# Performance work log

Measured on AMD Instinct MI355X. Metric: run time of the kernel, lower is better.

The kernel has to match this reference:

```python
import jax, jax.numpy as jnp
import numpy as np

B, S, IN, HID, NH, HD, R, WIN, TK = 2, 2048, 64, 512, 8, 64, 64, 5, 16
C1, C2, C3 = 171, 171, 170  # hidden_dim split across 3 conv branches (512 = 171+171+170)


def _conv(xc, w, b, pad):
    y = jax.lax.conv_general_dilated(xc, w, window_strides=(1,), padding=[(pad, pad)],
                                     dimension_numbers=('NCH', 'OIH', 'NCH'))
    return jax.nn.relu(y + b[None, :, None])


def setup_inputs():
    key = jax.random.key(0)
    ks = jax.random.split(key, 22)
    p = lambda k, sh: jax.random.normal(k, sh, jnp.float32) * 0.05
    return {
        'x': jax.random.normal(ks[0], (B, S, IN), jnp.float32),
        'conv1_w': p(ks[1], (C1, IN, 3)), 'conv1_b': p(ks[2], (C1,)),
        'conv2_w': p(ks[3], (C2, IN, 5)), 'conv2_b': p(ks[4], (C2,)),
        'conv3_w': p(ks[5], (C3, IN, 7)), 'conv3_b': p(ks[6], (C3,)),
        'Wq': p(ks[7], (HID, HID)), 'bq': p(ks[8], (HID,)),
        'Wk': p(ks[9], (HID, HID)), 'bk': p(ks[10], (HID,)),
        'Wv': p(ks[11], (HID, HID)), 'bv': p(ks[12], (HID,)),
        'Wkp': p(ks[13], (R, HD)), 'bkp': p(ks[14], (R,)),
        'Wvp': p(ks[15], (R, HD)), 'bvp': p(ks[16], (R,)),
        'Wo': p(ks[17], (HID, HID)), 'bo': p(ks[18], (HID,)),
        'ln_g': jnp.ones((HID,), jnp.float32), 'ln_b': jnp.zeros((HID,), jnp.float32),
    }


def reference(x, conv1_w, conv1_b, conv2_w, conv2_b, conv3_w, conv3_b,
              Wq, bq, Wk, bk, Wv, bv, Wkp, bkp, Wvp, bvp, Wo, bo, ln_g, ln_b):
    # multi-scale conv front-end
    xc = x.transpose(0, 2, 1)  # [B, IN, S]
    h = jnp.concatenate([_conv(xc, conv1_w, conv1_b, 1),
                         _conv(xc, conv2_w, conv2_b, 2),
                         _conv(xc, conv3_w, conv3_b, 3)], axis=1).transpose(0, 2, 1)  # [B,S,HID]

    def heads(W_, b_):
        return (h @ W_.T + b_).reshape(B, S, NH, HD).transpose(0, 2, 1, 3)  # [B,NH,S,HD]

    Q, K, V = heads(Wq, bq), heads(Wk, bk), heads(Wv, bv)
    Kp = K @ Wkp.T + bkp  # [B,NH,S,R]
    Vp = V @ Wvp.T + bvp

    # local sliding-window attention; -inf masking reproduces the per-t boundary slicing
    hw = WIN // 2
    idx = jnp.arange(S)[:, None] + jnp.arange(-hw, hw + 1)[None, :]
    valid = (idx >= 0) & (idx < S)
    idxc = jnp.clip(idx, 0, S - 1)
    Kw = K[:, :, idxc, :]
    Vw = V[:, :, idxc, :]
    ls = jnp.einsum('bhsd,bhswd->bhsw', Q, Kw) / jnp.sqrt(jnp.float32(HD))
    ls = jnp.where(valid[None, None], ls, -jnp.inf)
    local = jnp.einsum('bhsw,bhswd->bhsd', jax.nn.softmax(ls, axis=-1), Vw)

    # top-k low-rank global attention (HD == R required by original einsum)
    gs = jnp.einsum('bhqd,bhkd->bhqk', Q, Kp) / jnp.sqrt(jnp.float32(R))  # [B,NH,S,S]
    tv, ti = jax.lax.top_k(gs, TK)
    tw = jax.nn.softmax(tv, axis=-1)  # [B,NH,S,TK]
    bi = jnp.arange(B)[:, None, None, None]
    hi = jnp.arange(NH)[None, :, None, None]
    topV = Vp[bi, hi, ti]  # [B,NH,S,TK,R]
    sp = jnp.einsum('bhqk,bhqkr->bhqr', tw, topV)
    sp = sp @ Wvp.T + bvp  # extra value_proj applied to sparse output, as in original

    out = ((local + sp) * 0.5).transpose(0, 2, 1, 3).reshape(B, S, HID)
    out = out @ Wo.T + bo
    res = out + h
    mu = res.mean(-1, keepdims=True)
    var = ((res - mu) ** 2).mean(-1, keepdims=True)
    return (res - mu) / jnp.sqrt(var + 1e-5) * ln_g + ln_b
```

## Files before the change

kernel.cpp:

```cpp
#include <hip/hip_runtime.h>
#include <hip/hip_bf16.h>

#define BB 2
#define SS 2048
#define INC 64
#define HIDN 512
#define NHH 8
#define HDD 64
#define SP 2054

typedef __attribute__((ext_vector_type(8))) short bf16x8;
typedef __attribute__((ext_vector_type(4))) float f32x4;

__device__ __forceinline__ short f2bf(float f) {
  union { __hip_bfloat16 h; short s; } u;
  u.h = __float2bfloat16(f);
  return u.s;
}
__device__ __forceinline__ float bf2f(short s) {
  return __uint_as_float(((unsigned)(unsigned short)s) << 16);
}

__global__ __launch_bounds__(256) void prep_kernel(
    const float* __restrict__ x, const float* __restrict__ w1,
    const float* __restrict__ b1, const float* __restrict__ w2,
    const float* __restrict__ b2, const float* __restrict__ w3,
    const float* __restrict__ b3, const float* __restrict__ Wq,
    const float* __restrict__ Wk_, const float* __restrict__ Wv_,
    const float* __restrict__ bq, const float* __restrict__ bk_,
    const float* __restrict__ bv_, const float* __restrict__ Wo,
    const float* __restrict__ Wkp, const float* __restrict__ Wvp,
    const float* __restrict__ bvp, short* __restrict__ Wallbf,
    float* __restrict__ ball, short* __restrict__ Wobf,
    short* __restrict__ Wkpbf, short* __restrict__ W2bf,
    float* __restrict__ cvec, short* __restrict__ xbfp,
    short* __restrict__ Wcbf, float* __restrict__ bcat) {
  int i0 = blockIdx.x * 256 + threadIdx.x;
  int stride = gridDim.x * 256;
  for (int idx = i0; idx < 786432; idx += stride) {
    float v;
    if (idx < 262144)      v = Wq[idx];
    else if (idx < 524288) v = Wk_[idx - 262144];
    else                   v = Wv_[idx - 524288];
    Wallbf[idx] = f2bf(v);
  }
  for (int idx = i0; idx < 262144; idx += stride) Wobf[idx] = f2bf(Wo[idx]);
  for (int idx = i0; idx < BB * SP * 64; idx += stride) {
    int row = idx >> 6, ci = idx & 63;
    int b = row / SP, pr = row - b * SP;
    int sg = pr - 3;
    float v = (sg >= 0 && sg < SS) ? x[(b * SS + sg) * 64 + ci] : 0.f;
    xbfp[idx] = f2bf(v);
  }
  for (int idx = i0; idx < 512 * 448; idx += stride) {
    int c = idx / 448;
    int rem = idx - c * 448;
    int t = rem >> 6, ci = rem & 63;
    float v = 0.f;
    if (c < 171) {
      int k = t - 2;
      if (k >= 0 && k < 3) v = w1[(c * 64 + ci) * 3 + k];
    } else if (c < 342) {
      int k = t - 1;
      if (k >= 0 && k < 5) v = w2[((c - 171) * 64 + ci) * 5 + k];
    } else {
      v = w3[((c - 342) * 64 + ci) * 7 + t];
    }
    Wcbf[idx] = f2bf(v);
  }
  for (int idx = i0; idx < 4096; idx += stride) {
    Wkpbf[idx] = f2bf(Wkp[idx]);
    int j = idx >> 6, d = idx & 63;
    float s = 0.f;
#pragma unroll 8
    for (int i = 0; i < 64; i++) s += Wvp[j * 64 + i] * Wvp[i * 64 + d];
    W2bf[idx] = f2bf(s);
  }
  if (i0 < 1536) {
    float v;
    if (i0 < 512)       v = bq[i0];
    else if (i0 < 1024) v = bk_[i0 - 512];
    else                v = bv_[i0 - 1024];
    ball[i0] = v;
  }
  if (i0 < 512) {
    float v;
    if (i0 < 171)      v = b1[i0];
    else if (i0 < 342) v = b2[i0 - 171];
    else               v = b3[i0 - 342];
    bcat[i0] = v;
  }
  if (i0 < 64) {
    float s = bvp[i0];
#pragma unroll 8
    for (int i = 0; i < 64; i++) s += bvp[i] * Wvp[i0 * 64 + i];
    cvec[i0] = s;
  }
}

__global__ __launch_bounds__(256, 4) void gemm_conv(
    const short* __restrict__ xbfp, const short* __restrict__ Wcbf,
    const float* __restrict__ bcat, short* __restrict__ hbf) {
  int m0 = blockIdx.x * 128;
  int n0 = blockIdx.y * 64;
  int tid = threadIdx.x;
  int wvv = tid >> 6, lane = tid & 63;
  int quad = lane >> 4, l16 = lane & 15;
  int mw = m0 + wvv * 32;
  int r0 = mw + l16, r1 = r0 + 16;
  int b0 = r0 >> 11, s0 = r0 & 2047;
  int b1 = r1 >> 11, s1 = r1 & 2047;
  const short* ap0 = xbfp + (size_t)(b0 * SP + s0) * 64 + quad * 8;
  const short* ap1 = xbfp + (size_t)(b1 * SP + s1) * 64 + quad * 8;
  const short* bp = Wcbf + (size_t)(n0 + l16) * 448 + quad * 8;
  f32x4 acc[2][4] = {};
  bf16x8 cA0 = *(const bf16x8*)ap0;
  bf16x8 cA1 = *(const bf16x8*)ap1;
  bf16x8 cB0 = *(const bf16x8*)(bp + 0 * 16 * 448);
  bf16x8 cB1 = *(const bf16x8*)(bp + 1 * 16 * 448);
  bf16x8 cB2 = *(const bf16x8*)(bp + 2 * 16 * 448);
  bf16x8 cB3 = *(const bf16x8*)(bp + 3 * 16 * 448);
#pragma unroll 2
  for (int ks = 0; ks < 14; ks++) {
    int offn = (ks + 1 < 14 ? ks + 1 : 13) * 32;
    bf16x8 nA0 = *(const bf16x8*)(ap0 + offn);
    bf16x8 nA1 = *(const bf16x8*)(ap1 + offn);
    bf16x8 nB0 = *(const bf16x8*)(bp + 0 * 16 * 448 + offn);
    bf16x8 nB1 = *(const bf16x8*)(bp + 1 * 16 * 448 + offn);
    bf16x8 nB2 = *(const bf16x8*)(bp + 2 * 16 * 448 + offn);
    bf16x8 nB3 = *(const bf16x8*)(bp + 3 * 16 * 448 + offn);
    acc[0][0] = __builtin_amdgcn_mfma_f32_16x16x32_bf16(cA0, cB0, acc[0][0], 0, 0, 0);
    acc[1][0] = __builtin_amdgcn_mfma_f32_16x16x32_bf16(cA1, cB0, acc[1][0], 0, 0, 0);
    acc[0][1] = __builtin_amdgcn_mfma_f32_16x16x32_bf16(cA0, cB1, acc[0][1], 0, 0, 0);
    acc[1][1] = __builtin_amdgcn_mfma_f32_16x16x32_bf16(cA1, cB1, acc[1][1], 0, 0, 0);
    acc[0][2] = __builtin_amdgcn_mfma_f32_16x16x32_bf16(cA0, cB2, acc[0][2], 0, 0, 0);
    acc[1][2] = __builtin_amdgcn_mfma_f32_16x16x32_bf16(cA1, cB2, acc[1][2], 0, 0, 0);
    acc[0][3] = __builtin_amdgcn_mfma_f32_16x16x32_bf16(cA0, cB3, acc[0][3], 0, 0, 0);
    acc[1][3] = __builtin_amdgcn_mfma_f32_16x16x32_bf16(cA1, cB3, acc[1][3], 0, 0, 0);
    cA0 = nA0; cA1 = nA1;
    cB0 = nB0; cB1 = nB1; cB2 = nB2; cB3 = nB3;
  }
#pragma unroll
  for (int mt = 0; mt < 2; mt++) {
#pragma unroll
    for (int r = 0; r < 4; r++) {
      int m = mw + mt * 16 + quad * 4 + r;
#pragma unroll
      for (int t = 0; t < 4; t++) {
        int n = n0 + t * 16 + l16;
        float v = fmaxf(acc[mt][t][r] + bcat[n], 0.f);
        hbf[(size_t)m * 512 + n] = f2bf(v);
      }
    }
  }
}

__global__ __launch_bounds__(256, 4) void gemm_qkv(
    const short* __restrict__ Abf, const short* __restrict__ Wbf,
    const float* __restrict__ bias, short* __restrict__ Qh,
    short* __restrict__ Kh, short* __restrict__ Vh) {
  int m0 = blockIdx.x * 128;
  int n0 = blockIdx.y * 64;
  int tid = threadIdx.x;
  int wvv = tid >> 6, lane = tid & 63;
  int quad = lane >> 4, l16 = lane & 15;
  int mw = m0 + wvv * 32;
  const short* ap0 = Abf + (size_t)(mw + l16) * 512 + quad * 8;
  const short* ap1 = ap0 + 16 * 512;
  const short* bp = Wbf + (size_t)(n0 + l16) * 512 + quad * 8;
  f32x4 acc[2][4] = {};
  bf16x8 cA0 = *(const bf16x8*)ap0;
  bf16x8 cA1 = *(const bf16x8*)ap1;
  bf16x8 cB0 = *(const bf16x8*)(bp + 0 * 16 * 512);
  bf16x8 cB1 = *(const bf16x8*)(bp + 1 * 16 * 512);
  bf16x8 cB2 = *(const bf16x8*)(bp + 2 * 16 * 512);
  bf16x8 cB3 = *(const bf16x8*)(bp + 3 * 16 * 512);
#pragma unroll 2
  for (int ks = 0; ks < 16; ks++) {
    int offn = (ks + 1 < 16 ? ks + 1 : 15) * 32;
    bf16x8 nA0 = *(const bf16x8*)(ap0 + offn);
    bf16x8 nA1 = *(const bf16x8*)(ap1 + offn);
    bf16x8 nB0 = *(const bf16x8*)(bp + 0 * 16 * 512 + offn);
    bf16x8 nB1 = *(const bf16x8*)(bp + 1 * 16 * 512 + offn);
    bf16x8 nB2 = *(const bf16x8*)(bp + 2 * 16 * 512 + offn);
    bf16x8 nB3 = *(const bf16x8*)(bp + 3 * 16 * 512 + offn);
    acc[0][0] = __builtin_amdgcn_mfma_f32_16x16x32_bf16(cA0, cB0, acc[0][0], 0, 0, 0);
    acc[1][0] = __builtin_amdgcn_mfma_f32_16x16x32_bf16(cA1, cB0, acc[1][0], 0, 0, 0);
    acc[0][1] = __builtin_amdgcn_mfma_f32_16x16x32_bf16(cA0, cB1, acc[0][1], 0, 0, 0);
    acc[1][1] = __builtin_amdgcn_mfma_f32_16x16x32_bf16(cA1, cB1, acc[1][1], 0, 0, 0);
    acc[0][2] = __builtin_amdgcn_mfma_f32_16x16x32_bf16(cA0, cB2, acc[0][2], 0, 0, 0);
    acc[1][2] = __builtin_amdgcn_mfma_f32_16x16x32_bf16(cA1, cB2, acc[1][2], 0, 0, 0);
    acc[0][3] = __builtin_amdgcn_mfma_f32_16x16x32_bf16(cA0, cB3, acc[0][3], 0, 0, 0);
    acc[1][3] = __builtin_amdgcn_mfma_f32_16x16x32_bf16(cA1, cB3, acc[1][3], 0, 0, 0);
    cA0 = nA0; cA1 = nA1;
    cB0 = nB0; cB1 = nB1; cB2 = nB2; cB3 = nB3;
  }
  int which = n0 >> 9;
  int head = (n0 >> 6) & 7;
  short* dst = which == 0 ? Qh : (which == 1 ? Kh : Vh);
  float scale = which == 0 ? 0.125f : 1.0f;
#pragma unroll
  for (int mt = 0; mt < 2; mt++) {
#pragma unroll
    for (int r = 0; r < 4; r++) {
      int m = mw + mt * 16 + quad * 4 + r;
      int bb = m >> 11, s = m & 2047;
      size_t rowoff = ((size_t)(bb * 8 + head) * 2048 + s) * 64;
#pragma unroll
      for (int t = 0; t < 4; t++) {
        int hd = t * 16 + l16;
        float v = acc[mt][t][r] + bias[n0 + hd];
        dst[rowoff + hd] = f2bf(v * scale);
      }
    }
  }
}

__global__ __launch_bounds__(256, 4) void kpvp_local_kernel(
    const short* __restrict__ Kh, const short* __restrict__ Vh,
    const short* __restrict__ Wkpbf, const float* __restrict__ bkp,
    const short* __restrict__ W2bf, const float* __restrict__ cvec,
    short* __restrict__ Kfrag, float* __restrict__ Vpp,
    const short* __restrict__ Qh, float* __restrict__ ctxl) {
  int tid = threadIdx.x;
  __shared__ float Sloc[4][2][16][17];
  __shared__ float wloc[4][16][8];
  if (blockIdx.x < 256) {
    int m0 = blockIdx.x * 128;
    int wvv = tid >> 6, lane = tid & 63;
    int quad = lane >> 4, l16 = lane & 15;
    int mw = m0 + wvv * 32;
    {
      const short* ap0 = Kh + (size_t)(mw + l16) * 64 + quad * 8;
      const short* ap1 = ap0 + 16 * 64;
      const short* bp = Wkpbf + l16 * 64 + quad * 8;
      bf16x8 A00 = *(const bf16x8*)ap0, A01 = *(const bf16x8*)(ap0 + 32);
      bf16x8 A10 = *(const bf16x8*)ap1, A11 = *(const bf16x8*)(ap1 + 32);
      f32x4 acc[2][4] = {};
#pragma unroll
      for (int t = 0; t < 4; t++) {
        bf16x8 B0 = *(const bf16x8*)(bp + t * 16 * 64);
        bf16x8 B1 = *(const bf16x8*)(bp + t * 16 * 64 + 32);
        acc[0][t] = __builtin_amdgcn_mfma_f32_16x16x32_bf16(A00, B0, acc[0][t], 0, 0, 0);
        acc[0][t] = __builtin_amdgcn_mfma_f32_16x16x32_bf16(A01, B1, acc[0][t], 0, 0, 0);
        acc[1][t] = __builtin_amdgcn_mfma_f32_16x16x32_bf16(A10, B0, acc[1][t], 0, 0, 0);
        acc[1][t] = __builtin_amdgcn_mfma_f32_16x16x32_bf16(A11, B1, acc[1][t], 0, 0, 0);
      }
#pragma unroll
      for (int mt = 0; mt < 2; mt++)
#pragma unroll
        for (int r = 0; r < 4; r++) {
          int m = mw + mt * 16 + quad * 4 + r;
          int m15 = m & 15;
          size_t gbase = (size_t)(m >> 4) * 1024;
#pragma unroll
          for (int t = 0; t < 4; t++) {
            int n = t * 16 + l16;
            short val = f2bf(acc[mt][t][r] + bkp[n]);
            Kfrag[gbase + (size_t)(n >> 5) * 512 +
                  ((((n & 31) >> 3) * 16 + m15) << 3) + (n & 7)] = val;
          }
        }
    }
    {
      const short* ap0 = Vh + (size_t)(mw + l16) * 64 + quad * 8;
      const short* ap1 = ap0 + 16 * 64;
      const short* bp = W2bf + l16 * 64 + quad * 8;
      bf16x8 A00 = *(const bf16x8*)ap0, A01 = *(const bf16x8*)(ap0 + 32);
      bf16x8 A10 = *(const bf16x8*)ap1, A11 = *(const bf16x8*)(ap1 + 32);
      f32x4 acc[2][4] = {};
#pragma unroll
      for (int t = 0; t < 4; t++) {
        bf16x8 B0 = *(const bf16x8*)(bp + t * 16 * 64);
        bf16x8 B1 = *(const bf16x8*)(bp + t * 16 * 64 + 32);
        acc[0][t] = __builtin_amdgcn_mfma_f32_16x16x32_bf16(A00, B0, acc[0][t], 0, 0, 0);
        acc[0][t] = __builtin_amdgcn_mfma_f32_16x16x32_bf16(A01, B1, acc[0][t], 0, 0, 0);
        acc[1][t] = __builtin_amdgcn_mfma_f32_16x16x32_bf16(A10, B0, acc[1][t], 0, 0, 0);
        acc[1][t] = __builtin_amdgcn_mfma_f32_16x16x32_bf16(A11, B1, acc[1][t], 0, 0, 0);
      }
#pragma unroll
      for (int mt = 0; mt < 2; mt++)
#pragma unroll
        for (int r = 0; r < 4; r++) {
          int m = mw + mt * 16 + quad * 4 + r;
#pragma unroll
          for (int t = 0; t < 4; t++) {
            int n = t * 16 + l16;
            Vpp[(size_t)m * 64 + n] = acc[mt][t][r] + cvec[n];
          }
        }
    }
    return;
  }
  int wv = tid >> 6;
  int tile = (blockIdx.x - 256) * 4 + wv;
  int bh = tile >> 7;
  int q0 = (tile & 127) * 16;
  int lane = tid & 63;
  int quad = lane >> 4, l16 = lane & 15;

  const short* qbase = Qh + (size_t)(bh * 2048 + q0 + l16) * 64 + quad * 8;
  bf16x8 a0 = *(const bf16x8*)qbase;
  bf16x8 a1 = *(const bf16x8*)(qbase + 32);

  int k0a = min(max(q0 - 2 + l16, 0), 2047);
  int k1a = min(q0 + 6 + l16, 2047);
  const short* kb0 = Kh + (size_t)(bh * 2048 + k0a) * 64 + quad * 8;
  const short* kb1 = Kh + (size_t)(bh * 2048 + k1a) * 64 + quad * 8;
  bf16x8 B00 = *(const bf16x8*)kb0;
  bf16x8 B01 = *(const bf16x8*)(kb0 + 32);
  bf16x8 B10 = *(const bf16x8*)kb1;
  bf16x8 B11 = *(const bf16x8*)(kb1 + 32);
  f32x4 C0 = {0.f, 0.f, 0.f, 0.f};
  f32x4 C1 = {0.f, 0.f, 0.f, 0.f};
  C0 = __builtin_amdgcn_mfma_f32_16x16x32_bf16(a0, B00, C0, 0, 0, 0);
  C0 = __builtin_amdgcn_mfma_f32_16x16x32_bf16(a1, B01, C0, 0, 0, 0);
  C1 = __builtin_amdgcn_mfma_f32_16x16x32_bf16(a0, B10, C1, 0, 0, 0);
  C1 = __builtin_amdgcn_mfma_f32_16x16x32_bf16(a1, B11, C1, 0, 0, 0);
#pragma unroll
  for (int r = 0; r < 4; r++) {
    Sloc[wv][0][quad * 4 + r][l16] = C0[r];
    Sloc[wv][1][quad * 4 + r][l16] = C1[r];
  }
  __builtin_amdgcn_wave_barrier();
  if (lane < 16) {
    int q = lane;
    float sc[5];
    bool ok[5];
#pragma unroll
    for (int j = 0; j < 5; j++) {
      int offq = q + j - 2;
      int sg = q0 + offq;
      ok[j] = (sg >= 0 && sg < SS);
      int t = offq <= 13 ? 0 : 1;
      int col = t ? offq - 6 : offq + 2;
      sc[j] = ok[j] ? Sloc[wv][t][q][col] : -3.0e38f;
    }
    float m = -3.0e38f;
#pragma unroll
    for (int j = 0; j < 5; j++) m = fmaxf(m, sc[j]);
    float e[5], l = 0.f;
#pragma unroll
    for (int j = 0; j < 5; j++) {
      e[j] = ok[j] ? __expf(sc[j] - m) : 0.f;
      l += e[j];
    }
    float inv = 1.f / l;
#pragma unroll
    for (int j = 0; j < 5; j++) wloc[wv][q][j] = e[j] * inv;
  }
  __builtin_amdgcn_wave_barrier();
  {
    int q = lane >> 2, jb = (lane & 3) * 16;
    int s = q0 + q;
    float acc[16] = {};
#pragma unroll
    for (int j = 0; j < 5; j++) {
      int sg = s + j - 2;
      if (sg >= 0 && sg < SS) {
        float w = wloc[wv][q][j];
        const short* vr = Vh + (size_t)(bh * 2048 + sg) * 64 + jb;
#pragma unroll
        for (int u = 0; u < 16; u += 4) {
          short4 v4 = *(const short4*)(vr + u);
          acc[u + 0] += w * bf2f(v4.x);
          acc[u + 1] += w * bf2f(v4.y);
          acc[u + 2] += w * bf2f(v4.z);
          acc[u + 3] += w * bf2f(v4.w);
        }
      }
    }
    float* orow = ctxl + (size_t)(bh * 2048 + s) * 64 + jb;
#pragma unroll
    for (int u = 0; u < 16; u += 4)
      *(float4*)(orow + u) =
          make_float4(acc[u], acc[u + 1], acc[u + 2], acc[u + 3]);
  }
}

__global__ __launch_bounds__(256, 4) void global_attn(
    const short* __restrict__ Qh, const short* __restrict__ Kfrag,
    const float* __restrict__ Vpp, const float* __restrict__ ctxl,
    short* __restrict__ ctxcb) {
  int tid = threadIdx.x;
  int wv = tid >> 6;
  int lane = tid & 63;
  int quad = lane >> 4, l16 = lane & 15;
  int p = blockIdx.x;
  int bh = (p & 7) * 2 + ((p >> 3) & 1);
  int seg = p >> 4;
  int tile = seg * 4 + wv;
  int q0 = tile * 16;

  __shared__ float twl[4][16][17];
  __shared__ int   txl[4][16][17];

  const short* qbase = Qh + (size_t)(bh * 2048 + q0 + l16) * 64 + quad * 8;
  bf16x8 a0 = *(const bf16x8*)qbase;
  bf16x8 a1 = *(const bf16x8*)(qbase + 32);

  const short* kf = Kfrag + (size_t)bh * (128 * 1024) + lane * 8;

  unsigned er[4][8];
#pragma unroll
  for (int a = 0; a < 4; a++)
#pragma unroll
    for (int j = 0; j < 8; j++) er[a][j] = 0u;

  auto insert8 = [&](unsigned (&e)[8], unsigned cand) {
    unsigned n0, n1, n2, n3, n4, n5, n6, n7;
    asm("v_max_u32 %0, %1, %2" : "=v"(n0) : "v"(e[0]), "v"(cand));
    asm("v_med3_u32 %0, %1, %2, %3" : "=v"(n1) : "v"(e[0]), "v"(e[1]), "v"(cand));
    asm("v_med3_u32 %0, %1, %2, %3" : "=v"(n2) : "v"(e[1]), "v"(e[2]), "v"(cand));
    asm("v_med3_u32 %0, %1, %2, %3" : "=v"(n3) : "v"(e[2]), "v"(e[3]), "v"(cand));
    asm("v_med3_u32 %0, %1, %2, %3" : "=v"(n4) : "v"(e[3]), "v"(e[4]), "v"(cand));
    asm("v_med3_u32 %0, %1, %2, %3" : "=v"(n5) : "v"(e[4]), "v"(e[5]), "v"(cand));
    asm("v_med3_u32 %0, %1, %2, %3" : "=v"(n6) : "v"(e[5]), "v"(e[6]), "v"(cand));
    asm("v_med3_u32 %0, %1, %2, %3" : "=v"(n7) : "v"(e[6]), "v"(e[7]), "v"(cand));
    e[0] = n0; e[1] = n1; e[2] = n2; e[3] = n3;
    e[4] = n4; e[5] = n5; e[6] = n6; e[7] = n7;
  };
  auto mkcand = [&](float s, int idxr) -> unsigned {
    unsigned u = __float_as_uint(s);
    u ^= ((unsigned)((int)u >> 31)) | 0x80000000u;
    return (u & 0xFFFFF800u) | (unsigned)idxr;
  };

  int idxb = 2047 - l16;
#pragma unroll 4
  for (int g = 0; g < 128; g++) {
    bf16x8 B00 = *(const bf16x8*)(kf + g * 1024);
    bf16x8 B01 = *(const bf16x8*)(kf + g * 1024 + 512);
    f32x4 C0 = {0.f, 0.f, 0.f, 0.f};
    C0 = __builtin_amdgcn_mfma_f32_16x16x32_bf16(a0, B00, C0, 0, 0, 0);
    C0 = __builtin_amdgcn_mfma_f32_16x16x32_bf16(a1, B01, C0, 0, 0, 0);
    int idxr = idxb - (g << 4);
    insert8(er[0], mkcand(C0[0], idxr));
    insert8(er[1], mkcand(C0[1], idxr));
    insert8(er[2], mkcand(C0[2], idxr));
    insert8(er[3], mkcand(C0[3], idxr));
  }

  {
    float mval[4] = {0.f, 0.f, 0.f, 0.f};
    float lsum[4] = {0.f, 0.f, 0.f, 0.f};
    float myev[4] = {0.f, 0.f, 0.f, 0.f};
    int myki[4] = {0, 0, 0, 0};
#pragma unroll
    for (int t = 0; t < 16; t++) {
#pragma unroll
      for (int a = 0; a < 4; a++) {
        unsigned w = er[a][0];
#pragma unroll
        for (int mm = 1; mm <= 8; mm <<= 1) {
          unsigned o = (unsigned)__shfl_xor((int)w, mm);
          w = w > o ? w : o;
        }
        bool pop = (er[a][0] == w);
#pragma unroll
        for (int j = 0; j < 7; j++) er[a][j] = pop ? er[a][j + 1] : er[a][j];
        er[a][7] = pop ? 0u : er[a][7];
        unsigned wb = w & 0xFFFFF800u;
        unsigned uu = (w & 0x80000000u) ? (wb ^ 0x80000000u) : ~wb;
        float sv = (w == 0u) ? -1.0e30f : __uint_as_float(uu);
        if (t == 0) mval[a] = sv;
        float ex = __expf(sv - mval[a]);
        lsum[a] += ex;
        if (l16 == t) { myev[a] = ex; myki[a] = 2047 - (int)(w & 0x7FFu); }
      }
    }
#pragma unroll
    for (int a = 0; a < 4; a++) {
      twl[wv][quad * 4 + a][l16] = myev[a] / lsum[a];
      txl[wv][quad * 4 + a][l16] = myki[a];
    }
  }
  __builtin_amdgcn_wave_barrier();

  {
    int q = lane >> 2, d0 = (lane & 3) * 16;
    int b = bh >> 3, hh = bh & 7;
    const float* vball = Vpp + (size_t)bh * (2048 * 64) + d0;
    float acc[16];
#pragma unroll
    for (int u = 0; u < 16; u++) acc[u] = 0.f;
#pragma unroll 4
    for (int j = 0; j < 16; j++) {
      float w = twl[wv][q][j];
      const float* vr = vball + (size_t)txl[wv][q][j] * 64;
#pragma unroll
      for (int u = 0; u < 16; u += 4) {
        float4 v = *(const float4*)(vr + u);
        acc[u + 0] += w * v.x;
        acc[u + 1] += w * v.y;
        acc[u + 2] += w * v.z;
        acc[u + 3] += w * v.w;
      }
    }
    int s = q0 + q;
    const float* lrow = ctxl + (size_t)(bh * 2048 + s) * 64 + d0;
    short* orow = ctxcb + (size_t)(b * 2048 + s) * 512 + hh * 64 + d0;
#pragma unroll
    for (int u = 0; u < 16; u += 4) {
      float4 lv = *(const float4*)(lrow + u);
      short4 o;
      o.x = f2bf(0.5f * (lv.x + acc[u + 0]));
      o.y = f2bf(0.5f * (lv.y + acc[u + 1]));
      o.z = f2bf(0.5f * (lv.z + acc[u + 2]));
      o.w = f2bf(0.5f * (lv.w + acc[u + 3]));
      *(short4*)(orow + u) = o;
    }
  }
}

__global__ __launch_bounds__(256, 4) void gemm_wo(
    const short* __restrict__ Abf, const short* __restrict__ Wbf,
    const float* __restrict__ bo, const short* __restrict__ hbf,
    float* __restrict__ outp) {
  int m0 = blockIdx.x * 128;
  int n0 = blockIdx.y * 64;
  int tid = threadIdx.x;
  int wvv = tid >> 6, lane = tid & 63;
  int quad = lane >> 4, l16 = lane & 15;
  int mw = m0 + wvv * 32;
  const short* ap0 = Abf + (size_t)(mw + l16) * 512 + quad * 8;
  const short* ap1 = ap0 + 16 * 512;
  const short* bp = Wbf + (size_t)(n0 + l16) * 512 + quad * 8;
  f32x4 acc[2][4] = {};
  bf16x8 cA0 = *(const bf16x8*)ap0;
  bf16x8 cA1 = *(const bf16x8*)ap1;
  bf16x8 cB0 = *(const bf16x8*)(bp + 0 * 16 * 512);
  bf16x8 cB1 = *(const bf16x8*)(bp + 1 * 16 * 512);
  bf16x8 cB2 = *(const bf16x8*)(bp + 2 * 16 * 512);
  bf16x8 cB3 = *(const bf16x8*)(bp + 3 * 16 * 512);
#pragma unroll 2
  for (int ks = 0; ks < 16; ks++) {
    int offn = (ks + 1 < 16 ? ks + 1 : 15) * 32;
    bf16x8 nA0 = *(const bf16x8*)(ap0 + offn);
    bf16x8 nA1 = *(const bf16x8*)(ap1 + offn);
    bf16x8 nB0 = *(const bf16x8*)(bp + 0 * 16 * 512 + offn);
    bf16x8 nB1 = *(const bf16x8*)(bp + 1 * 16 * 512 + offn);
    bf16x8 nB2 = *(const bf16x8*)(bp + 2 * 16 * 512 + offn);
    bf16x8 nB3 = *(const bf16x8*)(bp + 3 * 16 * 512 + offn);
    acc[0][0] = __builtin_amdgcn_mfma_f32_16x16x32_bf16(cA0, cB0, acc[0][0], 0, 0, 0);
    acc[1][0] = __builtin_amdgcn_mfma_f32_16x16x32_bf16(cA1, cB0, acc[1][0], 0, 0, 0);
    acc[0][1] = __builtin_amdgcn_mfma_f32_16x16x32_bf16(cA0, cB1, acc[0][1], 0, 0, 0);
    acc[1][1] = __builtin_amdgcn_mfma_f32_16x16x32_bf16(cA1, cB1, acc[1][1], 0, 0, 0);
    acc[0][2] = __builtin_amdgcn_mfma_f32_16x16x32_bf16(cA0, cB2, acc[0][2], 0, 0, 0);
    acc[1][2] = __builtin_amdgcn_mfma_f32_16x16x32_bf16(cA1, cB2, acc[1][2], 0, 0, 0);
    acc[0][3] = __builtin_amdgcn_mfma_f32_16x16x32_bf16(cA0, cB3, acc[0][3], 0, 0, 0);
    acc[1][3] = __builtin_amdgcn_mfma_f32_16x16x32_bf16(cA1, cB3, acc[1][3], 0, 0, 0);
    cA0 = nA0; cA1 = nA1;
    cB0 = nB0; cB1 = nB1; cB2 = nB2; cB3 = nB3;
  }
#pragma unroll
  for (int mt = 0; mt < 2; mt++) {
#pragma unroll
    for (int r = 0; r < 4; r++) {
      int m = mw + mt * 16 + quad * 4 + r;
#pragma unroll
      for (int t = 0; t < 4; t++) {
        int n = n0 + t * 16 + l16;
        outp[(size_t)m * 512 + n] =
            acc[mt][t][r] + bo[n] + bf2f(hbf[(size_t)m * 512 + n]);
      }
    }
  }
}

__global__ __launch_bounds__(256) void ln_kernel(float* __restrict__ o,
                                                 const float* __restrict__ g,
                                                 const float* __restrict__ bb) {
  int row = blockIdx.x;
  int tid = threadIdx.x;
  float v0 = o[row * 512 + tid];
  float v1 = o[row * 512 + 256 + tid];
  float s = v0 + v1;
  float s2 = v0 * v0 + v1 * v1;
#pragma unroll
  for (int off = 1; off < 64; off <<= 1) {
    s += __shfl_xor(s, off);
    s2 += __shfl_xor(s2, off);
  }
  __shared__ float ps[4], ps2[4];
  int w = tid >> 6;
  if ((tid & 63) == 0) { ps[w] = s; ps2[w] = s2; }
  __syncthreads();
  float S = ps[0] + ps[1] + ps[2] + ps[3];
  float S2 = ps2[0] + ps2[1] + ps2[2] + ps2[3];
  float mu = S * (1.f / 512.f);
  float var = S2 * (1.f / 512.f) - mu * mu;
  float inv = rsqrtf(var + 1e-5f);
  o[row * 512 + tid] = (v0 - mu) * inv * g[tid] + bb[tid];
  o[row * 512 + 256 + tid] = (v1 - mu) * inv * g[tid + 256] + bb[tid + 256];
}

extern "C" void kernel_launch(void* const* d_in, const int* in_sizes, int n_in,
                              void* d_out, int out_size, void* d_ws,
                              size_t ws_size, hipStream_t stream) {
  const float* x   = (const float*)d_in[0];
  const float* w1  = (const float*)d_in[1];
  const float* b1  = (const float*)d_in[2];
  const float* w2  = (const float*)d_in[3];
  const float* b2  = (const float*)d_in[4];
  const float* w3  = (const float*)d_in[5];
  const float* b3  = (const float*)d_in[6];
  const float* Wq  = (const float*)d_in[7];
  const float* bq  = (const float*)d_in[8];
  const float* Wk  = (const float*)d_in[9];
  const float* bk  = (const float*)d_in[10];
  const float* Wv  = (const float*)d_in[11];
  const float* bv  = (const float*)d_in[12];
  const float* Wkp = (const float*)d_in[13];
  const float* bkp = (const float*)d_in[14];
  const float* Wvp = (const float*)d_in[15];
  const float* bvp = (const float*)d_in[16];
  const float* Wo  = (const float*)d_in[17];
  const float* bo  = (const float*)d_in[18];
  const float* lng = (const float*)d_in[19];
  const float* lnb = (const float*)d_in[20];

  float* p = (float*)d_ws;
  short* Wallbf = (short*)p;  p += 786432;
  float* ball   = p;          p += 2048;
  short* Wobf   = (short*)p;  p += 262144;
  short* Wkpbf  = (short*)p;  p += 4096;
  short* W2bf   = (short*)p;  p += 4096;
  float* cvec   = p;          p += 64;
  short* xbfp   = (short*)p;  p += 262912;
  short* Wcbf   = (short*)p;  p += 229376;
  float* bcat   = p;          p += 512;
  short* hbf    = (short*)p;  p += 1048576;
  short* Qh     = (short*)p;  p += 1048576;
  short* Kh     = (short*)p;  p += 1048576;
  short* Vh     = (short*)p;  p += 1048576;
  short* Kfrag  = (short*)p;  p += 1048576;
  float* Vpp    = p;          p += 2097152;
  float* ctxl   = p;          p += 2097152;
  short* ctxcb  = (short*)p;  p += 1048576;
  float* outF   = (float*)d_out;

  prep_kernel<<<512, 256, 0, stream>>>(x, w1, b1, w2, b2, w3, b3, Wq, Wk, Wv,
                                       bq, bk, bv, Wo, Wkp, Wvp, bvp, Wallbf,
                                       ball, Wobf, Wkpbf, W2bf, cvec, xbfp,
                                       Wcbf, bcat);
  {
    dim3 g(32, 8);
    gemm_conv<<<g, 256, 0, stream>>>(xbfp, Wcbf, bcat, hbf);
  }
  {
    dim3 g(32, 24);
    gemm_qkv<<<g, 256, 0, stream>>>(hbf, Wallbf, ball, Qh, Kh, Vh);
  }
  kpvp_local_kernel<<<768, 256, 0, stream>>>(Kh, Vh, Wkpbf, bkp, W2bf, cvec,
                                             Kfrag, Vpp, Qh, ctxl);
  global_attn<<<512, 256, 0, stream>>>(Qh, Kfrag, Vpp, ctxl, ctxcb);
  {
    dim3 g(32, 8);
    gemm_wo<<<g, 256, 0, stream>>>(ctxcb, Wobf, bo, hbf, outF);
  }
  ln_kernel<<<4096, 256, 0, stream>>>(outF, lng, lnb);
}
```

Measured before the change: 230.2 us.

## Split global top-k key scan across two waves per query tile and merge

Each query tile in global attention is now handled by two waves, each scanning half of the keys and keeping its own top-16. The two sorted lists are merged in shared memory by a small thread group that also computes the softmax, and the grid is doubled. The goal is to halve the serial per-wave key loop and add parallelism. The cost is extra block-wide syncs and a serial merge step run by only 32 threads. The bitonic-style merge (max of A[i] and B[15-i]) yields the top-16 set, but not in sorted order.

After: 230.4 us. About the same (+0.1%).

```diff
diff --git a/kernel.cpp b/kernel.cpp
--- a/kernel.cpp
+++ b/kernel.cpp
@@ -386,20 +386,24 @@
   int wv = tid >> 6;
   int lane = tid & 63;
   int quad = lane >> 4, l16 = lane & 15;
+  int tb = wv >> 1;
+  int half = wv & 1;
   int p = blockIdx.x;
   int bh = (p & 7) * 2 + ((p >> 3) & 1);
   int seg = p >> 4;
-  int tile = seg * 4 + wv;
+  int tile = seg * 2 + tb;
   int q0 = tile * 16;
 
-  __shared__ float twl[4][16][17];
-  __shared__ int   txl[4][16][17];
+  __shared__ unsigned swl[4][16][17];
+  __shared__ float twl[2][16][17];
+  __shared__ int   txl[2][16][17];
 
   const short* qbase = Qh + (size_t)(bh * 2048 + q0 + l16) * 64 + quad * 8;
   bf16x8 a0 = *(const bf16x8*)qbase;
   bf16x8 a1 = *(const bf16x8*)(qbase + 32);
 
-  const short* kf = Kfrag + (size_t)bh * (128 * 1024) + lane * 8;
+  const short* kf =
+      Kfrag + (size_t)bh * (128 * 1024) + (size_t)half * (64 * 1024) + lane * 8;
 
   unsigned er[4][8];
 #pragma unroll
@@ -426,9 +430,9 @@
     return (u & 0xFFFFF800u) | (unsigned)idxr;
   };
 
-  int idxb = 2047 - l16;
+  int idxb = 2047 - half * 1024 - l16;
 #pragma unroll 4
-  for (int g = 0; g < 128; g++) {
+  for (int g = 0; g < 64; g++) {
     bf16x8 B00 = *(const bf16x8*)(kf + g * 1024);
     bf16x8 B01 = *(const bf16x8*)(kf + g * 1024 + 512);
     f32x4 C0 = {0.f, 0.f, 0.f, 0.f};
@@ -442,10 +446,7 @@
   }
 
   {
-    float mval[4] = {0.f, 0.f, 0.f, 0.f};
-    float lsum[4] = {0.f, 0.f, 0.f, 0.f};
-    float myev[4] = {0.f, 0.f, 0.f, 0.f};
-    int myki[4] = {0, 0, 0, 0};
+    unsigned sw[4] = {0u, 0u, 0u, 0u};
 #pragma unroll
     for (int t = 0; t < 16; t++) {
 #pragma unroll
@@ -460,56 +461,85 @@
 #pragma unroll
         for (int j = 0; j < 7; j++) er[a][j] = pop ? er[a][j + 1] : er[a][j];
         er[a][7] = pop ? 0u : er[a][7];
-        unsigned wb = w & 0xFFFFF800u;
-        unsigned uu = (w & 0x80000000u) ? (wb ^ 0x80000000u) : ~wb;
-        float sv = (w == 0u) ? -1.0e30f : __uint_as_float(uu);
-        if (t == 0) mval[a] = sv;
-        float ex = __expf(sv - mval[a]);
-        lsum[a] += ex;
-        if (l16 == t) { myev[a] = ex; myki[a] = 2047 - (int)(w & 0x7FFu); }
+        if (l16 == t) sw[a] = w;
       }
     }
 #pragma unroll
-    for (int a = 0; a < 4; a++) {
-      twl[wv][quad * 4 + a][l16] = myev[a] / lsum[a];
-      txl[wv][quad * 4 + a][l16] = myki[a];
-    }
-  }
-  __builtin_amdgcn_wave_barrier();
+    for (int a = 0; a < 4; a++) swl[wv][quad * 4 + a][l16] = sw[a];
+  }
+  __syncthreads();
+
+  if (tid < 32) {
+    int tb2 = tid >> 4, q = tid & 15;
+    const unsigned* A = swl[tb2 * 2][q];
+    const unsigned* Bv = swl[tb2 * 2 + 1][q];
+    auto decode = [&](unsigned w) -> float {
+      unsigned wb = w & 0xFFFFF800u;
+      unsigned uu = (w & 0x80000000u) ? (wb ^ 0x80000000u) : ~wb;
+      return (w == 0u) ? -1.0e30f : __uint_as_float(uu);
+    };
+    unsigned h0 = A[0], h1 = Bv[0];
+    float mval = decode(h0 > h1 ? h0 : h1);
+    float lsum = 0.f;
+    float ev[16];
+    int ki[16];
+#pragma unroll
+    for (int i = 0; i < 16; i++) {
+      unsigned wa = A[i], wb2 = Bv[15 - i];
+      unsigned w = wa > wb2 ? wa : wb2;
+      float sv = decode(w);
+      float ex = __expf(sv - mval);
+      lsum += ex;
+      ev[i] = ex;
+      ki[i] = 2047 - (int)(w & 0x7FFu);
+    }
+    float inv = 1.f / lsum;
+#pragma unroll
+    for (int i = 0; i < 16; i++) {
+      twl[tb2][q][i] = ev[i] * inv;
+      txl[tb2][q][i] = ki[i];
+    }
+  }
+  __syncthreads();
 
   {
-    int q = lane >> 2, d0 = (lane & 3) * 16;
+    int tb2 = tid >> 7;
+    int r = tid & 127;
+    int q = r >> 3, d0 = (r & 7) * 8;
+    int tile2 = seg * 2 + tb2;
+    int q02 = tile2 * 16;
     int b = bh >> 3, hh = bh & 7;
     const float* vball = Vpp + (size_t)bh * (2048 * 64) + d0;
-    float acc[16];
-#pragma unroll
-    for (int u = 0; u < 16; u++) acc[u] = 0.f;
+    float acc[8];
+#pragma unroll
+    for (int u = 0; u < 8; u++) acc[u] = 0.f;
 #pragma unroll 4
     for (int j = 0; j < 16; j++) {
-      float w = twl[wv][q][j];
-      const float* vr = vball + (size_t)txl[wv][q][j] * 64;
-#pragma unroll
-      for (int u = 0; u < 16; u += 4) {
-        float4 v = *(const float4*)(vr + u);
-        acc[u + 0] += w * v.x;
-        acc[u + 1] += w * v.y;
-        acc[u + 2] += w * v.z;
-        acc[u + 3] += w * v.w;
-      }
-    }
-    int s = q0 + q;
+      float w = twl[tb2][q][j];
+      const float* vr = vball + (size_t)txl[tb2][q][j] * 64;
+      float4 v0 = *(const float4*)vr;
+      float4 v1 = *(const float4*)(vr + 4);
+      acc[0] += w * v0.x; acc[1] += w * v0.y;
+      acc[2] += w * v0.z; acc[3] += w * v0.w;
+      acc[4] += w * v1.x; acc[5] += w * v1.y;
+      acc[6] += w * v1.z; acc[7] += w * v1.w;
+    }
+    int s = q02 + q;
     const float* lrow = ctxl + (size_t)(bh * 2048 + s) * 64 + d0;
     short* orow = ctxcb + (size_t)(b * 2048 + s) * 512 + hh * 64 + d0;
-#pragma unroll
-    for (int u = 0; u < 16; u += 4) {
-      float4 lv = *(const float4*)(lrow + u);
-      short4 o;
-      o.x = f2bf(0.5f * (lv.x + acc[u + 0]));
-      o.y = f2bf(0.5f * (lv.y + acc[u + 1]));
-      o.z = f2bf(0.5f * (lv.z + acc[u + 2]));
-      o.w = f2bf(0.5f * (lv.w + acc[u + 3]));
-      *(short4*)(orow + u) = o;
-    }
+    float4 lv0 = *(const float4*)lrow;
+    float4 lv1 = *(const float4*)(lrow + 4);
+    short4 o0, o1;
+    o0.x = f2bf(0.5f * (lv0.x + acc[0]));
+    o0.y = f2bf(0.5f * (lv0.y + acc[1]));
+    o0.z = f2bf(0.5f * (lv0.z + acc[2]));
+    o0.w = f2bf(0.5f * (lv0.w + acc[3]));
+    o1.x = f2bf(0.5f * (lv1.x + acc[4]));
+    o1.y = f2bf(0.5f * (lv1.y + acc[5]));
+    o1.z = f2bf(0.5f * (lv1.z + acc[6]));
+    o1.w = f2bf(0.5f * (lv1.w + acc[7]));
+    *(short4*)orow = o0;
+    *(short4*)(orow + 4) = o1;
   }
 }
 
@@ -654,7 +684,7 @@
   }
   kpvp_local_kernel<<<768, 256, 0, stream>>>(Kh, Vh, Wkpbf, bkp, W2bf, cvec,
                                              Kfrag, Vpp, Qh, ctxl);
-  global_attn<<<512, 256, 0, stream>>>(Qh, Kfrag, Vpp, ctxl, ctxcb);
+  global_attn<<<1024, 256, 0, stream>>>(Qh, Kfrag, Vpp, ctxl, ctxcb);
   {
     dim3 g(32, 8);
     gemm_wo<<<g, 256, 0, stream>>>(ctxcb, Wobf, bo, hbf, outF);
```
